# Kernel optimization log

Hardware: AMD Instinct MI355X
Metric: run time of the kernel (lower is better)

Reference implementation:

```python
import jax, jax.numpy as jnp
import numpy as np

S, B, D, DV = 2048, 16, 128, 128


def setup_inputs() -> dict:
    key = jax.random.key(0)
    kq, kk, kv = jax.random.split(key, 3)
    return {
        "query": jax.random.normal(kq, (S, B, D), dtype=jnp.float32),
        "key": jax.random.normal(kk, (S, B, D), dtype=jnp.float32),
        "value": jax.random.normal(kv, (S, B, DV), dtype=jnp.float32),
    }


def reference(query, key, value):
    # sim: [B, S_q, S_k]
    d = key.shape[-1]
    sim = jnp.einsum('sbd,tbd->bst', query, key) / jnp.sqrt(jnp.asarray(d, query.dtype))
    # causal mask: disallow attending to future positions (strictly upper triangle)
    sq, sk = sim.shape[-2], sim.shape[-1]
    causal = jnp.tril(jnp.ones((sq, sk), dtype=bool))  # [S_q, S_k]
    sim = jnp.where(causal[None, :, :], sim, -jnp.inf)
    a = jax.nn.softmax(sim, axis=-1)  # dropout omitted (eval mode, p=0)
    # context: [S_q, B, D_v]
    context = jnp.einsum('bst,tbe->sbe', a, value)
    return context
```

## Files before the change

### kernel.cpp

```cpp
#include <hip/hip_runtime.h>
#include <stdint.h>

#define SS 2048
#define BB 16
#define DD 128
#define DVV 128
#define BQ 64
#define BK 32
#define NTILES (SS / BK)
#define TILE_HW 4096

typedef __attribute__((ext_vector_type(8))) short short8;
typedef __attribute__((ext_vector_type(4))) float float4v;

typedef __attribute__((address_space(1))) const void glob_cv;
typedef __attribute__((address_space(3))) void lds_v;

__device__ __forceinline__ short f2bf(float f) {
  union { float f; uint32_t u; } x;
  x.f = f;
  uint32_t r = x.u + 0x7fffu + ((x.u >> 16) & 1u);
  return (short)(r >> 16);
}

__device__ __forceinline__ int kappa(int quad, int j) {
  return (j < 4) ? (quad * 4 + j) : (16 + quad * 4 + (j - 4));
}

__global__ __launch_bounds__(256) void conv_kv(
    const float* __restrict__ kg, const float* __restrict__ vg,
    short* __restrict__ kimg, short* __restrict__ vimg) {
  __shared__ short tile[BK][136];
  const int t = blockIdx.x, b = blockIdx.y;
  const float* src_base = (blockIdx.z == 0) ? kg : vg;
  short* out = ((blockIdx.z == 0) ? kimg : vimg) + ((size_t)(b * NTILES + t)) * TILE_HW;
#pragma unroll
  for (int p = 0; p < 2; ++p) {
    const int ch = threadIdx.x + p * 256;
    const int key = ch >> 4, c = ch & 15;
    const float* src = src_base + ((size_t)(t * BK + key) * BB + b) * DD + c * 8;
    float4v f0 = *(const float4v*)src;
    float4v f1 = *(const float4v*)(src + 4);
    short8 s;
#pragma unroll
    for (int i = 0; i < 4; ++i) { s[i] = f2bf(f0[i]); s[4 + i] = f2bf(f1[i]); }
    *(short8*)&tile[key][c * 8] = s;
  }
  __syncthreads();
#pragma unroll
  for (int p = 0; p < 2; ++p) {
    const int idx = threadIdx.x + p * 256;
    const int j = idx >> 6, quad = (idx >> 4) & 3, mm = idx & 15;
    short8 s;
    if (blockIdx.z == 0) {
      const int ks = j >> 1, half = j & 1;
      s = *(const short8*)&tile[half * 16 + mm][(ks * 4 + quad) * 8];
    } else {
#pragma unroll
      for (int jj = 0; jj < 8; ++jj) s[jj] = tile[kappa(quad, jj)][j * 16 + mm];
    }
    *(short8*)(out + idx * 8) = s;
  }
}

__global__ __launch_bounds__(256) void attn_fwd(
    const float* __restrict__ qg, const short* __restrict__ kimg,
    const short* __restrict__ vimg, float* __restrict__ og) {
  __shared__ __align__(16) short smem[16 * 512];

  const int tid  = threadIdx.x;
  const int wave = tid >> 6;
  const int lane = tid & 63;
  const int m    = lane & 15;
  const int quad = lane >> 4;
  const int bid  = blockIdx.x;
  const int xcd = bid & 7;
  const int j   = bid >> 3;
  const int qt  = (j < 32) ? j : 63 - j;
  const int b   = 2 * xcd + (j >> 5);
  const int qw  = qt * BQ + wave * 16;
  const int qrow = qw + m;

  const float cscale = 0.08838834764831845f * 1.4426950408889634f;
  short8 qfrag[4];
#pragma unroll
  for (int ks = 0; ks < 4; ++ks) {
    const float* qp = qg + ((size_t)qrow * BB + b) * DD + ks * 32 + quad * 8;
    float4v f0 = *(const float4v*)qp;
    float4v f1 = *(const float4v*)(qp + 4);
    short8 f;
#pragma unroll
    for (int i = 0; i < 4; ++i) { f[i] = f2bf(f0[i] * cscale); f[4 + i] = f2bf(f1[i] * cscale); }
    qfrag[ks] = f;
  }

  float4v oacc[8];
#pragma unroll
  for (int i = 0; i < 8; ++i) oacc[i] = (float4v){0.f, 0.f, 0.f, 0.f};
  float psum = 0.f;

  const short* kbase = kimg + (size_t)b * NTILES * TILE_HW;
  const short* vbase = vimg + (size_t)b * NTILES * TILE_HW;
  const int cbase = wave * 4;
  const short* timg = (cbase < 8) ? kbase : vbase;
  const int coff = cbase & 7;

  const int ntile = 2 * qt + 2;

  for (int r = 0; r < ntile; ++r) {
    __syncthreads();
    {
      const short* src = timg + (size_t)r * TILE_HW + coff * 512 + lane * 8;
#pragma unroll
      for (int c = 0; c < 4; ++c)
        __builtin_amdgcn_global_load_lds((glob_cv*)(src + c * 512),
                                         (lds_v*)&smem[(cbase + c) * 512], 16, 0, 0);
    }
    __syncthreads();

    const short* kb = smem;
    const short* vb = smem + 8 * 512;

    float4v s0 = {0.f, 0.f, 0.f, 0.f}, s1 = {0.f, 0.f, 0.f, 0.f};
#pragma unroll
    for (int ks = 0; ks < 4; ++ks) {
      short8 kf0 = *(const short8*)(kb + (ks * 2 + 0) * 512 + lane * 8);
      short8 kf1 = *(const short8*)(kb + (ks * 2 + 1) * 512 + lane * 8);
      s0 = __builtin_amdgcn_mfma_f32_16x16x32_bf16(kf0, qfrag[ks], s0, 0, 0, 0);
      s1 = __builtin_amdgcn_mfma_f32_16x16x32_bf16(kf1, qfrag[ks], s1, 0, 0, 0);
    }
    float sv[8];
#pragma unroll
    for (int rr = 0; rr < 4; ++rr) { sv[rr] = s0[rr]; sv[4 + rr] = s1[rr]; }

    const int kt0 = r * BK;
    if (kt0 + BK - 1 > qw) {
#pragma unroll
      for (int jj = 0; jj < 8; ++jj)
        if (kt0 + kappa(quad, jj) > qrow) sv[jj] = -1e30f;
    }

    union { short8 s8; uint32_t w[4]; } pf;
#pragma unroll
    for (int jp = 0; jp < 4; ++jp) {
      float p0 = exp2f(sv[2 * jp]);
      float p1 = exp2f(sv[2 * jp + 1]);
      uint32_t w;
      asm("v_cvt_pk_bf16_f32 %0, %1, %2" : "=v"(w) : "v"(p0), "v"(p1));
      pf.w[jp] = w;
      union { uint32_t u; float f; } lo, hi;
      lo.u = w << 16;
      hi.u = w & 0xffff0000u;
      psum += lo.f;
      psum += hi.f;
    }
    const short8 pfrag = pf.s8;

#pragma unroll
    for (int nt = 0; nt < 8; ++nt) {
      short8 vf = *(const short8*)(vb + nt * 512 + lane * 8);
      oacc[nt] = __builtin_amdgcn_mfma_f32_16x16x32_bf16(pfrag, vf, oacc[nt], 0, 0, 0);
    }
  }

  float l = psum;
  l += __shfl_xor(l, 16, 64);
  l += __shfl_xor(l, 32, 64);
  const float linv = 1.0f / l;
  float l4[4];
#pragma unroll
  for (int rr = 0; rr < 4; ++rr) l4[rr] = __shfl(linv, quad * 4 + rr, 64);
#pragma unroll
  for (int rr = 0; rr < 4; ++rr) {
    const int qgl = qw + quad * 4 + rr;
    float* op = og + ((size_t)qgl * BB + b) * DVV + m;
#pragma unroll
    for (int nt = 0; nt < 8; ++nt) op[nt * 16] = oacc[nt][rr] * l4[rr];
  }
}

extern "C" void kernel_launch(void* const* d_in, const int* in_sizes, int n_in,
                              void* d_out, int out_size, void* d_ws, size_t ws_size,
                              hipStream_t stream) {
  const float* q = (const float*)d_in[0];
  const float* k = (const float*)d_in[1];
  const float* v = (const float*)d_in[2];
  float* out = (float*)d_out;
  short* kimg = (short*)d_ws;
  short* vimg = kimg + (size_t)BB * NTILES * TILE_HW;

  conv_kv<<<dim3(NTILES, BB, 2), 256, 0, stream>>>(k, v, kimg, vimg);
  attn_fwd<<<dim3(SS / BQ * BB), 256, 0, stream>>>(q, kimg, vimg, out);
}
```

Baseline: 146.8 us.

## Split KV tiles across two wave groups per block and merge partial outputs

Doubles the block to 512 threads. Two groups of four waves each process alternating KV tiles (even and odd) for the same 64 query rows, each into its own LDS buffer. The partial output accumulators and row sums are then merged through shared memory before the final normalisation. This halves the serial tile loop per wave and raises the number of waves in flight, at the cost of more LDS, a reduction step, and half the waves sitting idle during the epilogue.

```diff
diff --git a/kernel.cpp b/kernel.cpp
--- a/kernel.cpp
+++ b/kernel.cpp
@@ -63,13 +63,16 @@
   }
 }
 
-__global__ __launch_bounds__(256) void attn_fwd(
+__global__ __launch_bounds__(512) void attn_fwd(
     const float* __restrict__ qg, const short* __restrict__ kimg,
     const short* __restrict__ vimg, float* __restrict__ og) {
-  __shared__ __align__(16) short smem[16 * 512];
+  __shared__ __align__(16) char smem_raw[36864];
+  short* const sbuf = (short*)smem_raw;
 
   const int tid  = threadIdx.x;
   const int wave = tid >> 6;
+  const int par  = wave >> 2;
+  const int qsub = wave & 3;
   const int lane = tid & 63;
   const int m    = lane & 15;
   const int quad = lane >> 4;
@@ -78,7 +81,7 @@
   const int j   = bid >> 3;
   const int qt  = (j < 32) ? j : 63 - j;
   const int b   = 2 * xcd + (j >> 5);
-  const int qw  = qt * BQ + wave * 16;
+  const int qw  = qt * BQ + qsub * 16;
   const int qrow = qw + m;
 
   const float cscale = 0.08838834764831845f * 1.4426950408889634f;
@@ -101,25 +104,27 @@
 
   const short* kbase = kimg + (size_t)b * NTILES * TILE_HW;
   const short* vbase = vimg + (size_t)b * NTILES * TILE_HW;
-  const int cbase = wave * 4;
+  const int cbase = qsub * 4;
   const short* timg = (cbase < 8) ? kbase : vbase;
   const int coff = cbase & 7;
-
-  const int ntile = 2 * qt + 2;
-
-  for (int r = 0; r < ntile; ++r) {
+  short* const mybuf = sbuf + par * (16 * 512);
+
+  const int nround = qt + 1;
+
+  for (int r = 0; r < nround; ++r) {
+    const int t = 2 * r + par;
     __syncthreads();
     {
-      const short* src = timg + (size_t)r * TILE_HW + coff * 512 + lane * 8;
+      const short* src = timg + (size_t)t * TILE_HW + coff * 512 + lane * 8;
 #pragma unroll
       for (int c = 0; c < 4; ++c)
         __builtin_amdgcn_global_load_lds((glob_cv*)(src + c * 512),
-                                         (lds_v*)&smem[(cbase + c) * 512], 16, 0, 0);
+                                         (lds_v*)&mybuf[(cbase + c) * 512], 16, 0, 0);
     }
     __syncthreads();
 
-    const short* kb = smem;
-    const short* vb = smem + 8 * 512;
+    const short* kb = mybuf;
+    const short* vb = mybuf + 8 * 512;
 
     float4v s0 = {0.f, 0.f, 0.f, 0.f}, s1 = {0.f, 0.f, 0.f, 0.f};
 #pragma unroll
@@ -133,7 +138,7 @@
 #pragma unroll
     for (int rr = 0; rr < 4; ++rr) { sv[rr] = s0[rr]; sv[4 + rr] = s1[rr]; }
 
-    const int kt0 = r * BK;
+    const int kt0 = t * BK;
     if (kt0 + BK - 1 > qw) {
 #pragma unroll
       for (int jj = 0; jj < 8; ++jj)
@@ -163,19 +168,35 @@
     }
   }
 
-  float l = psum;
-  l += __shfl_xor(l, 16, 64);
-  l += __shfl_xor(l, 32, 64);
-  const float linv = 1.0f / l;
-  float l4[4];
-#pragma unroll
-  for (int rr = 0; rr < 4; ++rr) l4[rr] = __shfl(linv, quad * 4 + rr, 64);
-#pragma unroll
-  for (int rr = 0; rr < 4; ++rr) {
-    const int qgl = qw + quad * 4 + rr;
-    float* op = og + ((size_t)qgl * BB + b) * DVV + m;
-#pragma unroll
-    for (int nt = 0; nt < 8; ++nt) op[nt * 16] = oacc[nt][rr] * l4[rr];
+  __syncthreads();
+  float* const cw = (float*)smem_raw;
+  if (par == 1) {
+    float* p = cw + (size_t)(qsub * 64 + lane) * 36;
+#pragma unroll
+    for (int nt = 0; nt < 8; ++nt) *(float4v*)(p + nt * 4) = oacc[nt];
+    p[32] = psum;
+  }
+  __syncthreads();
+  if (par == 0) {
+    const float* p = cw + (size_t)(qsub * 64 + lane) * 36;
+#pragma unroll
+    for (int nt = 0; nt < 8; ++nt) oacc[nt] += *(const float4v*)(p + nt * 4);
+    psum += p[32];
+
+    float l = psum;
+    l += __shfl_xor(l, 16, 64);
+    l += __shfl_xor(l, 32, 64);
+    const float linv = 1.0f / l;
+    float l4[4];
+#pragma unroll
+    for (int rr = 0; rr < 4; ++rr) l4[rr] = __shfl(linv, quad * 4 + rr, 64);
+#pragma unroll
+    for (int rr = 0; rr < 4; ++rr) {
+      const int qgl = qw + quad * 4 + rr;
+      float* op = og + ((size_t)qgl * BB + b) * DVV + m;
+#pragma unroll
+      for (int nt = 0; nt < 8; ++nt) op[nt * 16] = oacc[nt][rr] * l4[rr];
+    }
   }
 }
 
@@ -190,5 +211,5 @@
   short* vimg = kimg + (size_t)BB * NTILES * TILE_HW;
 
   conv_kv<<<dim3(NTILES, BB, 2), 256, 0, stream>>>(k, v, kimg, vimg);
-  attn_fwd<<<dim3(SS / BQ * BB), 256, 0, stream>>>(q, kimg, vimg, out);
-}
+  attn_fwd<<<dim3(SS / BQ * BB), 512, 0, stream>>>(q, kimg, vimg, out);
+}
```

Result: faster. 136.3 us (-7.1%).
